# Kernel optimization log

Measured on AMD Instinct MI355X. Metric: run time of the kernel, lower is better.

Reference implementation:

```python
import jax, jax.numpy as jnp
import numpy as np

WS = 14      # window_size
NH = 12      # num_heads


def setup_inputs() -> dict:
    key = jax.random.key(0)
    k0, k1, k2 = jax.random.split(key, 3)
    B, H, W, C = 8, 56, 56, 768
    x = jax.random.normal(k0, (B, H * W, C), jnp.float32)
    s = 1.0 / np.sqrt(C).astype(np.float32)
    w_qkv = jax.random.normal(k1, (C, 3 * C), jnp.float32) * s   # qkv_bias=False
    w_proj = jax.random.normal(k2, (C, C), jnp.float32) * s
    b_proj = jnp.zeros((C,), jnp.float32)
    return {"x": x, "w_qkv": w_qkv, "w_proj": w_proj, "b_proj": b_proj, "H": H, "W": W}


def reference(x, w_qkv, w_proj, b_proj, H, W):
    ws, nh = WS, NH
    B, N, C = x.shape
    hd = C // nh
    H_ = -(-H // ws) * ws
    W_ = -(-W // ws) * ws
    Hn, Wn = H_ // ws, W_ // ws
    L, N_ = Hn * Wn, ws * ws

    qkv = x @ w_qkv                                   # [B, N, 3C]
    qkv = qkv.reshape(B, H, W, 3 * C)
    # pad AFTER the linear, as in the torch code (padded positions have qkv == 0)
    qkv = jnp.pad(qkv, ((0, 0), (0, H_ - H), (0, W_ - W), (0, 0)))
    # window partition: [B,Hn,ws,Wn,ws,3,nh,hd] -> [3,B,L,nh,N_,hd]
    qkv = qkv.reshape(B, Hn, ws, Wn, ws, 3, nh, hd)
    qkv = qkv.transpose(5, 0, 1, 3, 6, 2, 4, 7).reshape(3, B, L, nh, N_, hd)
    q, k, v = qkv[0], qkv[1], qkv[2]

    scale = hd ** -0.5
    attn = jnp.einsum('blhnd,blhmd->blhnm', q * scale, k)   # [B,L,nh,N_,N_]
    attn = jax.nn.softmax(attn, axis=-1)
    out = jnp.einsum('blhnm,blhmd->blhnd', attn, v)          # [B,L,nh,N_,hd]

    # fold windows back: -> [B,H_,W_,C], crop, flatten
    out = out.reshape(B, Hn, Wn, nh, ws, ws, hd)
    out = out.transpose(0, 1, 4, 2, 5, 3, 6).reshape(B, H_, W_, C)
    out = out[:, :H, :W].reshape(B, N, C)
    return out @ w_proj + b_proj
```

## Files before the change

kernel.cpp:

```cpp
#include <hip/hip_runtime.h>

typedef unsigned short u16;
typedef __attribute__((ext_vector_type(8))) __bf16 bf16x8;
typedef __attribute__((ext_vector_type(4))) float floatx4;

__device__ inline float bf2f(u16 u) {
  union { unsigned u; float f; } v; v.u = ((unsigned)u) << 16; return v.f;
}
__device__ inline u16 f2bf(float f) {
  union { float f; unsigned u; } v; v.f = f;
  unsigned r = v.u + 0x7fffu + ((v.u >> 16) & 1u);
  return (u16)(r >> 16);
}

__device__ inline void glds16(const u16* g, u16* l) {
  __builtin_amdgcn_global_load_lds((const __attribute__((address_space(1))) void*)g,
                                   (__attribute__((address_space(3))) void*)l, 16, 0, 0);
}

__global__ __launch_bounds__(256) void detect_k(const u16* __restrict__ w, int* flag)
{
  __shared__ int cnt;
  if (threadIdx.x == 0) cnt = 0;
  __syncthreads();
  int c = 0;
  for (int i = threadIdx.x; i < 16384; i += 256) {
    const int e = (w[i] >> 7) & 0xFF;
    if (e < 64 || e > 191) ++c;
  }
  atomicAdd(&cnt, c);
  __syncthreads();
  if (threadIdx.x == 0) *flag = (cnt > 256) ? 1 : 0;
}

__global__ __launch_bounds__(256) void cast_x_k(const void* __restrict__ in,
                                                u16* __restrict__ out,
                                                int n4, const int* __restrict__ flag)
{
  const int i = blockIdx.x * 256 + threadIdx.x;
  if (i >= n4) return;
  if (*flag) {
    const float4 v = ((const float4*)in)[i];
    u16 o0 = f2bf(v.x), o1 = f2bf(v.y), o2 = f2bf(v.z), o3 = f2bf(v.w);
    uint2 p; p.x = (unsigned)o0 | ((unsigned)o1 << 16); p.y = (unsigned)o2 | ((unsigned)o3 << 16);
    ((uint2*)out)[i] = p;
  } else {
    ((uint2*)out)[i] = ((const uint2*)in)[i];
  }
}

__global__ __launch_bounds__(256) void ct_transpose_k(const void* __restrict__ in,
                                                      u16* __restrict__ out,
                                                      int R, int C, const int* __restrict__ flag)
{
  __shared__ u16 tile[32][33];
  const int f = *flag;
  const int c0 = blockIdx.x * 32, r0 = blockIdx.y * 32;
  const int tx = threadIdx.x & 31, ty = threadIdx.x >> 5;
#pragma unroll
  for (int i = ty; i < 32; i += 8) {
    const size_t idx = (size_t)(r0 + i) * C + (c0 + tx);
    tile[i][tx] = f ? f2bf(((const float*)in)[idx]) : ((const u16*)in)[idx];
  }
  __syncthreads();
#pragma unroll
  for (int i = ty; i < 32; i += 8)
    out[(size_t)(c0 + i) * R + (r0 + tx)] = tile[tx][i];
}

__global__ __launch_bounds__(256) void bias_cast_k(const void* __restrict__ in,
                                                   float* __restrict__ out,
                                                   int n, const int* __restrict__ flag)
{
  const int i = blockIdx.x * 256 + threadIdx.x;
  if (i >= n) return;
  out[i] = *flag ? ((const float*)in)[i] : bf2f(((const u16*)in)[i]);
}

__global__ __launch_bounds__(256) void gemm_bt(
    const u16* __restrict__ A, const u16* __restrict__ Bt,
    const float* __restrict__ bias, void* __restrict__ C,
    int M, int N, int K, const int* __restrict__ flag, int flagOut)
{
  __shared__ u16 smem[8192];
  u16* As = smem;
  u16* Bs = smem + 4096;
  const int t = threadIdx.x;
  const int wave = t >> 6, lane = t & 63;
  const int quad = lane >> 4, l15 = lane & 15;
  const int wr = (wave >> 1) << 6, wc = (wave & 1) << 6;
  const size_t m0 = (size_t)blockIdx.x * 128;
  const size_t n0 = (size_t)blockIdx.y * 128;

  const int sgk = (((t & 3) ^ ((t >> 3) & 3))) * 8;
  const u16* ag0 = A + (m0 + (t >> 2)) * (size_t)K + sgk;
  const u16* ag1 = ag0 + (size_t)64 * K;
  const u16* bg0 = Bt + (n0 + (t >> 2)) * (size_t)K + sgk;
  const u16* bg1 = bg0 + (size_t)64 * K;
  u16* la = As + wave * 512;
  u16* lb = Bs + wave * 512;

  const int kx = (l15 >> 1) & 3;
  const int xq = (quad ^ kx) * 8;

  floatx4 acc[4][4] = {};

  for (int k0 = 0; k0 < K; k0 += 32) {
    glds16(ag0 + k0, la);
    glds16(ag1 + k0, la + 2048);
    glds16(bg0 + k0, lb);
    glds16(bg1 + k0, lb + 2048);
    __syncthreads();
    bf16x8 af[4], bfv[4];
#pragma unroll
    for (int i = 0; i < 4; ++i)
      af[i] = *(const bf16x8*)(As + (wr + i * 16 + l15) * 32 + xq);
#pragma unroll
    for (int j = 0; j < 4; ++j)
      bfv[j] = *(const bf16x8*)(Bs + (wc + j * 16 + l15) * 32 + xq);
#pragma unroll
    for (int i = 0; i < 4; ++i)
#pragma unroll
      for (int j = 0; j < 4; ++j)
        acc[i][j] = __builtin_amdgcn_mfma_f32_16x16x32_bf16(af[i], bfv[j], acc[i][j], 0, 0, 0);
    __syncthreads();
  }

  float bvj[4];
#pragma unroll
  for (int j = 0; j < 4; ++j)
    bvj[j] = bias ? bias[n0 + wc + j * 16 + l15] : 0.0f;

  if (flagOut && (*flag)) {
    float* scrf = (float*)smem + wave * 576;
    float* Cf = (float*)C;
#pragma unroll
    for (int i = 0; i < 4; ++i)
#pragma unroll
      for (int jp = 0; jp < 2; ++jp) {
#pragma unroll
        for (int jj = 0; jj < 2; ++jj)
#pragma unroll
          for (int r = 0; r < 4; ++r)
            scrf[(quad * 4 + r) * 36 + jj * 16 + l15] = acc[i][jp * 2 + jj][r] + bvj[jp * 2 + jj];
#pragma unroll
        for (int u = lane; u < 128; u += 64) {
          const int row = u >> 3, gr = u & 7;
          float4 vv = *(const float4*)(scrf + row * 36 + gr * 4);
          *(float4*)(Cf + (m0 + wr + i * 16 + row) * (size_t)N + n0 + wc + jp * 32 + gr * 4) = vv;
        }
      }
  } else {
    u16* scr = smem + wave * 1152;
    u16* Cb = (u16*)C;
#pragma unroll
    for (int i = 0; i < 4; ++i) {
#pragma unroll
      for (int j = 0; j < 4; ++j)
#pragma unroll
        for (int r = 0; r < 4; ++r)
          scr[(quad * 4 + r) * 72 + j * 16 + l15] = f2bf(acc[i][j][r] + bvj[j]);
#pragma unroll
      for (int u = lane; u < 128; u += 64) {
        const int row = u >> 3, gr = u & 7;
        int4 vv = *(const int4*)(scr + row * 72 + gr * 8);
        *(int4*)(Cb + (m0 + wr + i * 16 + row) * (size_t)N + n0 + wc + gr * 8) = vv;
      }
    }
  }
}

__global__ __launch_bounds__(256, 2) void attn_win(
    const u16* __restrict__ qkv, u16* __restrict__ o)
{
  __shared__ u16 Ks[196 * 64];
  __shared__ u16 Vt[64 * 208];
  __shared__ u16 Pb[4][16 * 208];
  __shared__ int gtok[208];

  const int bid = blockIdx.x;
  const int h = bid % 12;
  const int l = (bid / 12) % 16;
  const int b = bid / 192;
  const int wr0 = (l >> 2) * 14, wc0 = (l & 3) * 14;
  const int baseTok = b * 3136;

  const int t = threadIdx.x, wave = t >> 6, lane = t & 63;
  const int quad = lane >> 4, l15 = lane & 15;

  if (t < 208) {
    const int nn = t < 196 ? t : 195;
    gtok[t] = baseTok + (wr0 + nn / 14) * 56 + wc0 + nn % 14;
  }
  __syncthreads();

  for (int u = t; u < 196 * 8; u += 256) {
    const int row = u >> 3, gg = u & 7;
    int4 kv = *(const int4*)(qkv + (size_t)gtok[row] * 2304 + 768 + h * 64 + gg * 8);
    *(int4*)(Ks + (row * 8 + (gg ^ (row & 7))) * 8) = kv;
  }
  for (int u = t; u < 208 * 8; u += 256) {
    const int n = u >> 3, dg = u & 7;
    int4 vv = {0, 0, 0, 0};
    if (n < 196)
      vv = *(const int4*)(qkv + (size_t)gtok[n] * 2304 + 1536 + h * 64 + dg * 8);
    const u16* pv = (const u16*)&vv;
#pragma unroll
    for (int j = 0; j < 8; ++j) Vt[(dg * 8 + j) * 208 + n] = pv[j];
  }
  __syncthreads();

  u16* Pw = &Pb[wave][0];
  const bf16x8 zerov = {};

  for (int rt = wave; rt < 13; rt += 4) {
    const int n0r = rt * 16;
    int qn = n0r + l15; if (qn > 195) qn = 195;
    const u16* qrow = qkv + (size_t)gtok[qn] * 2304 + h * 64;
    const bf16x8 aq0 = *(const bf16x8*)(qrow + quad * 8);
    const bf16x8 aq1 = *(const bf16x8*)(qrow + 32 + quad * 8);

    floatx4 s[13];
#pragma unroll
    for (int ct = 0; ct < 13; ++ct) {
      int kr = ct * 16 + l15; if (kr > 195) kr = 195;
      const bf16x8 bk0 = *(const bf16x8*)(Ks + (kr * 8 + (quad ^ (kr & 7))) * 8);
      const bf16x8 bk1 = *(const bf16x8*)(Ks + (kr * 8 + ((quad + 4) ^ (kr & 7))) * 8);
      floatx4 z = {};
      z = __builtin_amdgcn_mfma_f32_16x16x32_bf16(aq0, bk0, z, 0, 0, 0);
      z = __builtin_amdgcn_mfma_f32_16x16x32_bf16(aq1, bk1, z, 0, 0, 0);
      s[ct] = z;
    }

    float mx[4], sm[4];
#pragma unroll
    for (int r = 0; r < 4; ++r) mx[r] = -3e38f;
#pragma unroll
    for (int ct = 0; ct < 13; ++ct) {
      const bool maskct = (ct == 12) && (l15 >= 4);
#pragma unroll
      for (int r = 0; r < 4; ++r) {
        float v = s[ct][r] * 0.125f;
        if (maskct) v = -3e38f;
        s[ct][r] = v;
        mx[r] = fmaxf(mx[r], v);
      }
    }
#pragma unroll
    for (int r = 0; r < 4; ++r)
      for (int off = 1; off < 16; off <<= 1)
        mx[r] = fmaxf(mx[r], __shfl_xor(mx[r], off, 64));
#pragma unroll
    for (int r = 0; r < 4; ++r) sm[r] = 0.0f;
#pragma unroll
    for (int ct = 0; ct < 13; ++ct)
#pragma unroll
      for (int r = 0; r < 4; ++r) {
        const float p = __expf(s[ct][r] - mx[r]);
        s[ct][r] = p;
        sm[r] += p;
      }
#pragma unroll
    for (int r = 0; r < 4; ++r)
      for (int off = 1; off < 16; off <<= 1)
        sm[r] += __shfl_xor(sm[r], off, 64);

#pragma unroll
    for (int ct = 0; ct < 13; ++ct)
#pragma unroll
      for (int r = 0; r < 4; ++r)
        Pw[(quad * 4 + r) * 208 + ct * 16 + l15] = f2bf(s[ct][r]);

    floatx4 oacc[4] = {};
#pragma unroll
    for (int ks = 0; ks < 6; ++ks) {
      const bf16x8 ap = *(const bf16x8*)(Pw + l15 * 208 + ks * 32 + quad * 8);
#pragma unroll
      for (int nt = 0; nt < 4; ++nt) {
        const bf16x8 bv = *(const bf16x8*)(Vt + (nt * 16 + l15) * 208 + ks * 32 + quad * 8);
        oacc[nt] = __builtin_amdgcn_mfma_f32_16x16x32_bf16(ap, bv, oacc[nt], 0, 0, 0);
      }
    }
    {
      const int off = 192 + (quad & 1) * 8;
      bf16x8 ap = *(const bf16x8*)(Pw + l15 * 208 + off);
      if (quad >= 2) ap = zerov;
#pragma unroll
      for (int nt = 0; nt < 4; ++nt) {
        const bf16x8 bv = *(const bf16x8*)(Vt + (nt * 16 + l15) * 208 + off);
        oacc[nt] = __builtin_amdgcn_mfma_f32_16x16x32_bf16(ap, bv, oacc[nt], 0, 0, 0);
      }
    }

    float rs[4];
#pragma unroll
    for (int r = 0; r < 4; ++r) rs[r] = 1.0f / sm[r];

#pragma unroll
    for (int nt = 0; nt < 4; ++nt)
#pragma unroll
      for (int r = 0; r < 4; ++r)
        Pw[(quad * 4 + r) * 208 + nt * 16 + l15] = f2bf(oacc[nt][r] * rs[r]);
#pragma unroll
    for (int u = lane; u < 128; u += 64) {
      const int row = u >> 3, gr = u & 7;
      const int n = n0r + row;
      if (n < 196) {
        int4 vv = *(const int4*)(Pw + row * 208 + gr * 8);
        *(int4*)(o + (size_t)gtok[n] * 768 + h * 64 + gr * 8) = vv;
      }
    }
  }
}

extern "C" void kernel_launch(void* const* d_in, const int* in_sizes, int n_in,
                              void* d_out, int out_size, void* d_ws, size_t ws_size,
                              hipStream_t stream)
{
  const void* x     = d_in[0];
  const void* wqkv  = d_in[1];
  const void* wproj = d_in[2];
  const void* bproj = d_in[3];

  char* ws = (char*)d_ws;
  int*   flag   = (int*)ws;
  float* bprojF = (float*)(ws + 16);
  u16*   wqkvT  = (u16*)(ws + 4096);
  u16*   wprojT = (u16*)(ws + 3543040);
  u16*   qkvbuf = (u16*)(ws + 4722688);
  u16*   xb     = (u16*)(ws + 120328192);
  u16*   attno  = xb;

  detect_k<<<1, 256, 0, stream>>>((const u16*)wqkv, flag);
  cast_x_k<<<dim3(18816), 256, 0, stream>>>(x, xb, 4816896, flag);
  ct_transpose_k<<<dim3(72, 24), 256, 0, stream>>>(wqkv, wqkvT, 768, 2304, flag);
  ct_transpose_k<<<dim3(24, 24), 256, 0, stream>>>(wproj, wprojT, 768, 768, flag);
  bias_cast_k<<<dim3(3), 256, 0, stream>>>(bproj, bprojF, 768, flag);

  gemm_bt<<<dim3(196, 18), 256, 0, stream>>>(xb, wqkvT, (const float*)nullptr, qkvbuf,
                                             25088, 2304, 768, flag, 0);
  attn_win<<<dim3(1536), 256, 0, stream>>>(qkvbuf, attno);
  gemm_bt<<<dim3(196, 6), 256, 0, stream>>>(attno, wprojT, bprojF, d_out,
                                            25088, 768, 768, flag, 1);
}
```

Before: 443.8 us.

## Double GEMM K-step to 64 with new swizzle and grouped tile rasterization

The bf16 GEMM now stages a 64-wide K slice per iteration instead of 32, using an 8-way XOR swizzle in LDS. This halves the number of barrier-separated iterations and issues twice as many MFMAs per sync. Blocks are launched on a 1D grid and remapped so that groups of 14 M-tiles sweep all N-tiles together, to improve L2 reuse of the A and B tiles. LDS usage doubles to 32 KB per block, which may lower occupancy.

Result: faster. 402.6 us (-9.3%).

```diff
diff --git a/kernel.cpp b/kernel.cpp
--- a/kernel.cpp
+++ b/kernel.cpp
@@ -80,49 +80,55 @@
 __global__ __launch_bounds__(256) void gemm_bt(
     const u16* __restrict__ A, const u16* __restrict__ Bt,
     const float* __restrict__ bias, void* __restrict__ C,
-    int M, int N, int K, const int* __restrict__ flag, int flagOut)
-{
-  __shared__ u16 smem[8192];
+    int M, int N, int K, const int* __restrict__ flag, int flagOut, int NT)
+{
+  __shared__ u16 smem[16384];
   u16* As = smem;
-  u16* Bs = smem + 4096;
+  u16* Bs = smem + 8192;
   const int t = threadIdx.x;
   const int wave = t >> 6, lane = t & 63;
   const int quad = lane >> 4, l15 = lane & 15;
   const int wr = (wave >> 1) << 6, wc = (wave & 1) << 6;
-  const size_t m0 = (size_t)blockIdx.x * 128;
-  const size_t n0 = (size_t)blockIdx.y * 128;
-
-  const int sgk = (((t & 3) ^ ((t >> 3) & 3))) * 8;
-  const u16* ag0 = A + (m0 + (t >> 2)) * (size_t)K + sgk;
-  const u16* ag1 = ag0 + (size_t)64 * K;
-  const u16* bg0 = Bt + (n0 + (t >> 2)) * (size_t)K + sgk;
-  const u16* bg1 = bg0 + (size_t)64 * K;
+
+  const int id = blockIdx.x;
+  const int grp = id / (14 * NT), rem = id % (14 * NT);
+  const int mt = grp * 14 + rem % 14;
+  const int ntile = rem / 14;
+  const size_t m0 = (size_t)mt * 128;
+  const size_t n0 = (size_t)ntile * 128;
+
+  const int srow = wave * 8 + (lane >> 3);
+  const int sg = ((lane & 7) ^ (lane >> 3)) * 8;
+  const u16* ag = A + (m0 + srow) * (size_t)K + sg;
+  const u16* bg = Bt + (n0 + srow) * (size_t)K + sg;
   u16* la = As + wave * 512;
   u16* lb = Bs + wave * 512;
 
-  const int kx = (l15 >> 1) & 3;
-  const int xq = (quad ^ kx) * 8;
-
   floatx4 acc[4][4] = {};
 
-  for (int k0 = 0; k0 < K; k0 += 32) {
-    glds16(ag0 + k0, la);
-    glds16(ag1 + k0, la + 2048);
-    glds16(bg0 + k0, lb);
-    glds16(bg1 + k0, lb + 2048);
+  for (int k0 = 0; k0 < K; k0 += 64) {
+#pragma unroll
+    for (int w = 0; w < 4; ++w) glds16(ag + k0 + (size_t)(w * 32) * K, la + w * 2048);
+#pragma unroll
+    for (int w = 0; w < 4; ++w) glds16(bg + k0 + (size_t)(w * 32) * K, lb + w * 2048);
     __syncthreads();
-    bf16x8 af[4], bfv[4];
-#pragma unroll
-    for (int i = 0; i < 4; ++i)
-      af[i] = *(const bf16x8*)(As + (wr + i * 16 + l15) * 32 + xq);
-#pragma unroll
-    for (int j = 0; j < 4; ++j)
-      bfv[j] = *(const bf16x8*)(Bs + (wc + j * 16 + l15) * 32 + xq);
-#pragma unroll
-    for (int i = 0; i < 4; ++i)
+#pragma unroll
+    for (int ks = 0; ks < 2; ++ks) {
+      bf16x8 af[4], bfv[4];
+      const int gf = ks * 4 + quad;
+      const int slot = (gf ^ (l15 & 7)) * 8;
+#pragma unroll
+      for (int i = 0; i < 4; ++i)
+        af[i] = *(const bf16x8*)(As + (wr + i * 16 + l15) * 64 + slot);
 #pragma unroll
       for (int j = 0; j < 4; ++j)
-        acc[i][j] = __builtin_amdgcn_mfma_f32_16x16x32_bf16(af[i], bfv[j], acc[i][j], 0, 0, 0);
+        bfv[j] = *(const bf16x8*)(Bs + (wc + j * 16 + l15) * 64 + slot);
+#pragma unroll
+      for (int i = 0; i < 4; ++i)
+#pragma unroll
+        for (int j = 0; j < 4; ++j)
+          acc[i][j] = __builtin_amdgcn_mfma_f32_16x16x32_bf16(af[i], bfv[j], acc[i][j], 0, 0, 0);
+    }
     __syncthreads();
   }
 
@@ -337,9 +343,9 @@
   ct_transpose_k<<<dim3(24, 24), 256, 0, stream>>>(wproj, wprojT, 768, 768, flag);
   bias_cast_k<<<dim3(3), 256, 0, stream>>>(bproj, bprojF, 768, flag);
 
-  gemm_bt<<<dim3(196, 18), 256, 0, stream>>>(xb, wqkvT, (const float*)nullptr, qkvbuf,
-                                             25088, 2304, 768, flag, 0);
+  gemm_bt<<<dim3(196 * 18), 256, 0, stream>>>(xb, wqkvT, (const float*)nullptr, qkvbuf,
+                                              25088, 2304, 768, flag, 0, 18);
   attn_win<<<dim3(1536), 256, 0, stream>>>(qkvbuf, attno);
-  gemm_bt<<<dim3(196, 6), 256, 0, stream>>>(attno, wprojT, bprojF, d_out,
-                                            25088, 768, 768, flag, 1);
-}
+  gemm_bt<<<dim3(196 * 6), 256, 0, stream>>>(attno, wprojT, bprojF, d_out,
+                                             25088, 768, 768, flag, 1, 6);
+}
```
